# Performance work log

Hardware: AMD Instinct MI355X
Metric: run time of the kernel (lower is better)

The kernel has to match this reference:

```python
import jax, jax.numpy as jnp
import numpy as np

GRID_SIZE = 5
SPLINE_ORDER = 3


def b_splines(x):
    """Cox-de Boor B-spline bases. x: [N, in] -> [N, in, GRID_SIZE+SPLINE_ORDER]."""
    k = SPLINE_ORDER
    h = 2.0 / GRID_SIZE  # grid range [-1, 1]
    grid = jnp.arange(-k, GRID_SIZE + k + 1, dtype=x.dtype) * h - 1.0  # [G+2k+1]
    xe = x[..., None]  # [N, in, 1]
    b = ((xe >= grid[:-1]) & (xe < grid[1:])).astype(x.dtype)
    for j in range(1, k + 1):
        b = ((xe - grid[:-(j + 1)]) / (grid[j:-1] - grid[:-(j + 1)]) * b[..., :-1]
             + (grid[j + 1:] - xe) / (grid[j + 1:] - grid[1:-j]) * b[..., 1:])
    return b  # [N, in, G+k]


def kan_linear(x, base_w, spline_w):
    """efficient-KAN KANLinear: silu base branch + spline branch.
    x: [N, in], base_w: [out, in], spline_w: [out, in, G+k] -> [N, out]."""
    base = jnp.einsum('ni,oi->no', jax.nn.silu(x), base_w)
    spline = jnp.einsum('nig,oig->no', b_splines(x), spline_w)
    return base + spline


def setup_inputs() -> dict:
    key = jax.random.key(0)
    ks = jax.random.split(key, 8)
    C, R, G = 128, 8, GRID_SIZE + SPLINE_ORDER  # in_channels, reduced, n_bases
    B, H, W, D = 2, 64, 64, 64
    s = 0.1  # keep spline weights in a sane init range
    return {
        'x': jax.random.normal(ks[0], (B, C, H, W, D), dtype=jnp.float32),
        'ck1_base': jax.random.normal(ks[1], (R, C), dtype=jnp.float32) * s,
        'ck1_spline': jax.random.normal(ks[2], (R, C, G), dtype=jnp.float32) * s,
        'ck2_base': jax.random.normal(ks[3], (C, R), dtype=jnp.float32) * s,
        'ck2_spline': jax.random.normal(ks[4], (C, R, G), dtype=jnp.float32) * s,
        'conv_w': jax.random.normal(ks[5], (C,), dtype=jnp.float32) * 0.1,
        'sk_base': jax.random.normal(ks[6], (1, 1), dtype=jnp.float32),
        'sk_spline': jax.random.normal(ks[7], (1, 1, G), dtype=jnp.float32),
    }


def reference(x, ck1_base, ck1_spline, ck2_base, ck2_spline, conv_w, sk_base, sk_spline):
    B, C, H, W, D = x.shape
    # channel attention: avg/max pool -> KAN -> ReLU -> KAN, shared weights
    y_avg = jnp.mean(x, axis=(2, 3, 4))  # [B, C]
    y_max = jnp.max(x, axis=(2, 3, 4))   # [B, C]

    def channel_mlp(y):
        h1 = jax.nn.relu(kan_linear(y, ck1_base, ck1_spline))
        return kan_linear(h1, ck2_base, ck2_spline)

    channel_att = jax.nn.sigmoid(channel_mlp(y_avg) + channel_mlp(y_max))
    x_channel = x * channel_att[:, :, None, None, None]

    # spatial attention: 1x1x1 conv (C->1, no bias) then per-voxel 1->1 KAN
    y_spatial = jnp.einsum('bchwd,c->bhwd', x_channel, conv_w)
    y_flat = y_spatial.reshape(-1, 1)  # [B*H*W*D, 1]
    spatial_att = jax.nn.sigmoid(kan_linear(y_flat, sk_base, sk_spline))
    spatial_att = spatial_att.reshape(B, 1, H, W, D)
    return x_channel * spatial_att
```

## Files before the change

### kernel.cpp

```cpp
#include <hip/hip_runtime.h>
#include <math.h>

#define HWD 262144
#define C_CH 128
#define B_N 2
#define VT 128
#define K3_BLOCKS 256
#define K3_TILES 16

typedef float f4 __attribute__((ext_vector_type(4)));

__device__ __forceinline__ float sigmoidf_(float v) {
    return 1.0f / (1.0f + expf(-v));
}

__device__ __forceinline__ void bspline8(float x, float* bs) {
    float g[12];
#pragma unroll
    for (int i = 0; i < 12; ++i) g[i] = (float)(i - 3) * 0.4f - 1.0f;
    float b[11];
#pragma unroll
    for (int t = 0; t < 11; ++t) b[t] = (x >= g[t] && x < g[t + 1]) ? 1.0f : 0.0f;
#pragma unroll
    for (int j = 1; j <= 3; ++j) {
#pragma unroll
        for (int t = 0; t + j < 11; ++t) {
            b[t] = (x - g[t]) / (g[t + j] - g[t]) * b[t]
                 + (g[t + j + 1] - x) / (g[t + j + 1] - g[t + 1]) * b[t + 1];
        }
    }
#pragma unroll
    for (int t = 0; t < 8; ++t) bs[t] = b[t];
}

__global__ __launch_bounds__(1024) void k1_pool(const float* __restrict__ x,
                                                float* __restrict__ ws) {
    int bid = blockIdx.x;
    const float4* xp = (const float4*)(x + (size_t)bid * HWD);
    int tid = threadIdx.x;
    float s = 0.0f, m = -INFINITY;
#pragma unroll 4
    for (int i = 0; i < 64; ++i) {
        float4 v = xp[(size_t)i * 1024 + tid];
        s += (v.x + v.y) + (v.z + v.w);
        m = fmaxf(m, fmaxf(fmaxf(v.x, v.y), fmaxf(v.z, v.w)));
    }
#pragma unroll
    for (int off = 32; off > 0; off >>= 1) {
        s += __shfl_xor(s, off, 64);
        m = fmaxf(m, __shfl_xor(m, off, 64));
    }
    __shared__ float ssum[16], smax[16];
    int wave = tid >> 6, lane = tid & 63;
    if (lane == 0) { ssum[wave] = s; smax[wave] = m; }
    __syncthreads();
    if (tid == 0) {
        float S = 0.0f, M = -INFINITY;
#pragma unroll
        for (int w = 0; w < 16; ++w) { S += ssum[w]; M = fmaxf(M, smax[w]); }
        ws[bid]       = S / (float)HWD;
        ws[256 + bid] = M;
    }
}

__global__ __launch_bounds__(1024) void k3_fused(
    const float* __restrict__ x, const float* __restrict__ ws,
    const float* __restrict__ ck1_base, const float* __restrict__ ck1_spline,
    const float* __restrict__ ck2_base, const float* __restrict__ ck2_spline,
    const float* __restrict__ conv_w,
    const float* __restrict__ sk_base, const float* __restrict__ sk_spline,
    float* __restrict__ out) {
    __shared__ __align__(16) float xs[2][C_CH * VT];
    __shared__ float scratch[512 * 8];
    __shared__ __align__(16) float satt[VT];
    __shared__ float catts[B_N][C_CH];
    __shared__ float w2s[B_N][C_CH];
    __shared__ float h1silu[32];
    __shared__ float h1bs[32][8];
    __shared__ float out2[512];

    int tid = threadIdx.x;
    int bid = blockIdx.x;

    f4 rg[4];
    {
        const float* xb = x + ((size_t)bid << 7);
#pragma unroll
        for (int m = 0; m < 4; ++m) {
            int f = m * 1024 + tid;
            int c = f >> 5, j = f & 31;
            rg[m] = *(const f4*)(xb + (size_t)c * HWD + j * 4);
        }
    }

    if (tid < 512) {
        int pool = tid >> 8, b = (tid >> 7) & 1, i = tid & 127;
        float v = ws[pool * 256 + b * 128 + i];
        float sv = v * sigmoidf_(v);
        float bsv[8];
        bspline8(v, bsv);
#pragma unroll
        for (int r = 0; r < 8; ++r) {
            float acc = sv * ck1_base[r * 128 + i];
#pragma unroll
            for (int g = 0; g < 8; ++g)
                acc += bsv[g] * ck1_spline[(r * 128 + i) * 8 + g];
            scratch[tid * 8 + r] = acc;
        }
    }
    __syncthreads();
    if (tid < 32) {
        int pool = tid >> 4, b = (tid >> 3) & 1, r = tid & 7;
        int tb = pool * 256 + b * 128;
        float acc = 0.0f;
        for (int i = 0; i < 128; ++i) acc += scratch[(tb + i) * 8 + r];
        float h = fmaxf(acc, 0.0f);
        h1silu[tid] = h * sigmoidf_(h);
        bspline8(h, h1bs[tid]);
    }
    __syncthreads();
    if (tid < 512) {
        int pool = tid >> 8, b = (tid >> 7) & 1, o = tid & 127;
        float acc = 0.0f;
#pragma unroll
        for (int r = 0; r < 8; ++r) {
            int hidx = pool * 16 + b * 8 + r;
            acc += h1silu[hidx] * ck2_base[o * 8 + r];
#pragma unroll
            for (int g = 0; g < 8; ++g)
                acc += h1bs[hidx][g] * ck2_spline[(o * 8 + r) * 8 + g];
        }
        out2[tid] = acc;
    }
    __syncthreads();
    if (tid < 256) {
        int b = tid >> 7, o = tid & 127;
        float catt = sigmoidf_(out2[b * 128 + o] + out2[256 + b * 128 + o]);
        catts[b][o] = catt;
        w2s[b][o]   = catt * conv_w[o];
    }
#pragma unroll
    for (int m = 0; m < 4; ++m) {
        int f = m * 1024 + tid;
        int c = f >> 5, j = f & 31;
        *(f4*)&xs[0][c * VT + j * 4] = rg[m];
    }
    __syncthreads();

    int buf = 0;
    for (int it = 0; it < K3_TILES; ++it) {
        int b  = it >> 3;
        int v0 = (((it & 7) << 8) + bid) << 7;
        float* ob = out + (size_t)b * C_CH * HWD + v0;

        f4 rn[4];
        int itn = it + 1;
        if (itn < K3_TILES) {
            int bn  = itn >> 3;
            int v0n = (((itn & 7) << 8) + bid) << 7;
            const float* xbn = x + (size_t)bn * C_CH * HWD + v0n;
#pragma unroll
            for (int m = 0; m < 4; ++m) {
                int f = m * 1024 + tid;
                int c = f >> 5, j = f & 31;
                rn[m] = *(const f4*)(xbn + (size_t)c * HWD + j * 4);
            }
        }

        {
            int v = tid & (VT - 1), q = tid >> 7;
            float acc = 0.0f;
#pragma unroll
            for (int cc = 0; cc < 16; ++cc) {
                int c = q * 16 + cc;
                acc += xs[buf][c * VT + v] * w2s[b][c];
            }
            scratch[tid] = acc;
        }
        __syncthreads();
        if (tid < VT) {
            float s = 0.0f;
#pragma unroll
            for (int k = 0; k < 8; ++k) s += scratch[tid + k * 128];
            float bs[8];
            bspline8(s, bs);
            float a = s * sigmoidf_(s) * sk_base[0];
#pragma unroll
            for (int g = 0; g < 8; ++g) a += bs[g] * sk_spline[g];
            satt[tid] = sigmoidf_(a);
        }
        __syncthreads();
#pragma unroll
        for (int m = 0; m < 4; ++m) {
            int f = m * 1024 + tid;
            int c = f >> 5, j = f & 31;
            f4 vv = *(f4*)&xs[buf][c * VT + j * 4];
            f4 sa = *(f4*)&satt[j * 4];
            float ca = catts[b][c];
            f4 o = vv * ca * sa;
            __builtin_nontemporal_store(o, (f4*)(ob + (size_t)c * HWD + j * 4));
        }
        if (itn < K3_TILES) {
            int nb = buf ^ 1;
#pragma unroll
            for (int m = 0; m < 4; ++m) {
                int f = m * 1024 + tid;
                int c = f >> 5, j = f & 31;
                *(f4*)&xs[nb][c * VT + j * 4] = rn[m];
            }
            buf = nb;
        }
        __syncthreads();
    }
}

extern "C" void kernel_launch(void* const* d_in, const int* in_sizes, int n_in,
                              void* d_out, int out_size, void* d_ws, size_t ws_size,
                              hipStream_t stream) {
    const float* x          = (const float*)d_in[0];
    const float* ck1_base   = (const float*)d_in[1];
    const float* ck1_spline = (const float*)d_in[2];
    const float* ck2_base   = (const float*)d_in[3];
    const float* ck2_spline = (const float*)d_in[4];
    const float* conv_w     = (const float*)d_in[5];
    const float* sk_base    = (const float*)d_in[6];
    const float* sk_spline  = (const float*)d_in[7];
    float* out = (float*)d_out;
    float* ws  = (float*)d_ws;

    k1_pool<<<B_N * C_CH, 1024, 0, stream>>>(x, ws);
    k3_fused<<<K3_BLOCKS, 1024, 0, stream>>>(x, ws, ck1_base, ck1_spline,
                                             ck2_base, ck2_spline, conv_w,
                                             sk_base, sk_spline, out);
}
```

Measured before the change: 492.8 us.

## Keep x tiles in registers instead of double-buffered LDS staging

Removes the 128KB double-buffered shared-memory copy of each x tile and keeps the tile in registers. The channel dot product is computed from registers with a padded transposed scratch reduction, and the output is written from the same registers. This cuts LDS traffic, one barrier per tile and the shared-memory footprint, which may allow more overlap. In exchange, the reduction now goes through a 32-way serial sum per voxel.

```diff
diff --git a/kernel.cpp b/kernel.cpp
--- a/kernel.cpp
+++ b/kernel.cpp
@@ -70,8 +70,7 @@
     const float* __restrict__ conv_w,
     const float* __restrict__ sk_base, const float* __restrict__ sk_spline,
     float* __restrict__ out) {
-    __shared__ __align__(16) float xs[2][C_CH * VT];
-    __shared__ float scratch[512 * 8];
+    __shared__ float scratch[4224];
     __shared__ __align__(16) float satt[VT];
     __shared__ float catts[B_N][C_CH];
     __shared__ float w2s[B_N][C_CH];
@@ -81,14 +80,15 @@
 
     int tid = threadIdx.x;
     int bid = blockIdx.x;
+    int col = tid >> 5;
+    int j   = tid & 31;
 
     f4 rg[4];
     {
         const float* xb = x + ((size_t)bid << 7);
 #pragma unroll
         for (int m = 0; m < 4; ++m) {
-            int f = m * 1024 + tid;
-            int c = f >> 5, j = f & 31;
+            int c = m * 32 + col;
             rg[m] = *(const f4*)(xb + (size_t)c * HWD + j * 4);
         }
     }
@@ -139,15 +139,8 @@
         catts[b][o] = catt;
         w2s[b][o]   = catt * conv_w[o];
     }
-#pragma unroll
-    for (int m = 0; m < 4; ++m) {
-        int f = m * 1024 + tid;
-        int c = f >> 5, j = f & 31;
-        *(f4*)&xs[0][c * VT + j * 4] = rg[m];
-    }
-    __syncthreads();
-
-    int buf = 0;
+    __syncthreads();
+
     for (int it = 0; it < K3_TILES; ++it) {
         int b  = it >> 3;
         int v0 = (((it & 7) << 8) + bid) << 7;
@@ -161,27 +154,24 @@
             const float* xbn = x + (size_t)bn * C_CH * HWD + v0n;
 #pragma unroll
             for (int m = 0; m < 4; ++m) {
-                int f = m * 1024 + tid;
-                int c = f >> 5, j = f & 31;
+                int c = m * 32 + col;
                 rn[m] = *(const f4*)(xbn + (size_t)c * HWD + j * 4);
             }
         }
 
-        {
-            int v = tid & (VT - 1), q = tid >> 7;
-            float acc = 0.0f;
-#pragma unroll
-            for (int cc = 0; cc < 16; ++cc) {
-                int c = q * 16 + cc;
-                acc += xs[buf][c * VT + v] * w2s[b][c];
-            }
-            scratch[tid] = acc;
+#pragma unroll
+        for (int k = 0; k < 4; ++k) {
+            float p = rg[0][k] * w2s[b][col]
+                    + rg[1][k] * w2s[b][32 + col]
+                    + rg[2][k] * w2s[b][64 + col]
+                    + rg[3][k] * w2s[b][96 + col];
+            scratch[(j * 4 + k) * 33 + col] = p;
         }
         __syncthreads();
         if (tid < VT) {
             float s = 0.0f;
 #pragma unroll
-            for (int k = 0; k < 8; ++k) s += scratch[tid + k * 128];
+            for (int q = 0; q < 32; ++q) s += scratch[tid * 33 + q];
             float bs[8];
             bspline8(s, bs);
             float a = s * sigmoidf_(s) * sk_base[0];
@@ -190,27 +180,17 @@
             satt[tid] = sigmoidf_(a);
         }
         __syncthreads();
+        f4 sa = *(f4*)&satt[j * 4];
 #pragma unroll
         for (int m = 0; m < 4; ++m) {
-            int f = m * 1024 + tid;
-            int c = f >> 5, j = f & 31;
-            f4 vv = *(f4*)&xs[buf][c * VT + j * 4];
-            f4 sa = *(f4*)&satt[j * 4];
-            float ca = catts[b][c];
-            f4 o = vv * ca * sa;
+            int c = m * 32 + col;
+            f4 o = rg[m] * catts[b][c] * sa;
             __builtin_nontemporal_store(o, (f4*)(ob + (size_t)c * HWD + j * 4));
         }
         if (itn < K3_TILES) {
-            int nb = buf ^ 1;
-#pragma unroll
-            for (int m = 0; m < 4; ++m) {
-                int f = m * 1024 + tid;
-                int c = f >> 5, j = f & 31;
-                *(f4*)&xs[nb][c * VT + j * 4] = rn[m];
-            }
-            buf = nb;
-        }
-        __syncthreads();
+#pragma unroll
+            for (int m = 0; m < 4; ++m) rg[m] = rn[m];
+        }
     }
 }
 
```

Result: no change. 494.6 us (+0.4%).
